# Kernel tuning notes

Measured on AMD Instinct MI355X. Metric: run time of the kernel, lower is better.

Reference implementation:

```python
import jax, jax.numpy as jnp
from jax import lax
import numpy as np

NSTART, NOPEN, NHID, NCLOSE, NLAYERS, KSZ, N = 40, 128, 256, 3, 40, 9, 1024
H_STEP = 0.1
PAD = (KSZ - 1) // 2  # 4 -> same-length conv
EPS = 1e-5


def conv1(x, K):
    # x: (1, Cin, N), K: (Cout, Cin, k); cross-correlation like torch F.conv1d
    return lax.conv_general_dilated(x, K, (1,), [(PAD, PAD)],
                                    dimension_numbers=('NCH', 'OIH', 'NCH'))


def conv1T(x, K):
    # torch F.conv_transpose1d(x, K, padding=PAD) == conv1d with swapped-channel,
    # flipped kernel and padding k-1-PAD (= PAD here since k=9, PAD=4)
    Kt = jnp.flip(jnp.swapaxes(K, 0, 1), -1)
    return lax.conv_general_dilated(x, Kt, (1,), [(PAD, PAD)],
                                    dimension_numbers=('NCH', 'OIH', 'NCH'))


def instance_norm(x):
    # x: (1, C, N); normalize per channel over spatial dim, biased var, no affine
    m = jnp.mean(x, axis=-1, keepdims=True)
    v = jnp.var(x, axis=-1, keepdims=True)
    return (x - m) * lax.rsqrt(v + EPS)


def get_graph_lap(Z):
    # Z: (C, N). Normalized Gaussian-affinity graph Laplacian.
    sq = jnp.sum(Z * Z, axis=0)  # (N,)
    D2 = jnp.maximum(sq[:, None] + sq[None, :] - 2.0 * (Z.T @ Z), 0.0)
    sigma = jnp.mean(D2) + 1e-12
    Wg = jnp.exp(-D2 / sigma)
    deg = jnp.sum(Wg, axis=1)
    Dh = lax.rsqrt(deg)
    L = Dh[:, None] * (jnp.diag(deg) - Wg) * Dh[None, :]
    return L, deg


def double_sym_layer(Z, Wi, Bi, L):
    # Z: (nopen, N), Wi: (2, nhid, nopen, 9), Bi: (2, nopen, 1), L: (N, N)
    A0 = instance_norm(conv1((Z + Bi[0])[None], Wi[0]))
    A1 = instance_norm((conv1((Z + Bi[1])[None], Wi[1])[0] @ L)[None])
    A0 = jax.nn.relu(A0)
    A1 = jax.nn.relu(A1)
    A0 = conv1T(A0, Wi[0])[0]
    A1 = conv1T(A1, Wi[1])[0] @ L.T
    return A0 + A1  # (nopen, N)


def setup_inputs() -> dict:
    key = jax.random.key(0)
    k1, k2, k3, k4, k5 = jax.random.split(key, 5)
    Z = jax.random.normal(k1, (NSTART, N), dtype=jnp.float32)
    stdv_o = 0.001 * NOPEN / NSTART
    Kopen = jax.random.uniform(k2, (NOPEN, NSTART), minval=-stdv_o, maxval=stdv_o, dtype=jnp.float32)
    stdv_c = 0.001 * NCLOSE / NOPEN
    Kclose = jax.random.uniform(k3, (NCLOSE, NOPEN), minval=-stdv_c, maxval=stdv_c, dtype=jnp.float32)
    W = jax.random.uniform(k4, (NLAYERS, 2, NHID, NOPEN, KSZ), minval=-1e-4, maxval=1e-4, dtype=jnp.float32)
    Bias = jax.random.uniform(k5, (NLAYERS, 2, NOPEN, 1), dtype=jnp.float32) * 1e-4
    return {"Z": Z, "Kopen": Kopen, "Kclose": Kclose, "W": W, "Bias": Bias}


def reference(Z, Kopen, Kclose, W, Bias):
    h = H_STEP
    Zc = Kopen @ Z          # (nopen, N)
    Zold = Zc
    L, _ = get_graph_lap(Zc)
    for i in range(NLAYERS):
        if i % 10 == 0:
            L, _ = get_graph_lap(Zc)
        Ai = double_sym_layer(Zc, W[i], Bias[i], L)
        Zc, Zold = 2.0 * Zc - Zold - (h * h) * Ai, Zc  # leapfrog step
    return (Kclose @ Zc, Kclose @ Zold)
```

## Files before the change

kernel.cpp:

```cpp
#include <hip/hip_runtime.h>

#define NN 1024
#define NOPEN 128
#define NHID 256
#define NSTART 40
#define NCLOSE 3
#define NLAYERS 40
#define KSZ 9

static constexpr float H2 = 0.01f;
static constexpr float IN_EPS = 1e-5f;

using floatx4 = __attribute__((ext_vector_type(4))) float;
using bfrag = __attribute__((ext_vector_type(8))) short;

__device__ __forceinline__ ushort f2bf(float f) {
    union { float f; unsigned u; } v; v.f = f;
    unsigned r = v.u + 0x7fffu + ((v.u >> 16) & 1u);
    return (ushort)(r >> 16);
}

__device__ __forceinline__ void prepw_piece(const float* __restrict__ W, ushort* __restrict__ Wt,
                                            ushort* __restrict__ WtT, int lb, int lsrc, int tid) {
    if (lb < 72) {
        int q = lb; int coq = q & 3; q >>= 2; int t = q % 9, z = q / 9;
        const float* Wz = W + (size_t)(lsrc * 2 + z) * (NHID * NOPEN * KSZ);
        ushort* Wo = Wt + ((size_t)z * 9 + t) * (NHID * NOPEN);
#pragma unroll
        for (int r = 0; r < 32; ++r) {
            int idx = r * 256 + tid;
            int co = coq * 64 + (idx >> 7), ci = idx & 127;
            Wo[co * NOPEN + ci] = f2bf(Wz[co * (NOPEN * KSZ) + ci * KSZ + t]);
        }
    } else {
        int q = lb - 72; int ciq = q & 3; q >>= 2; int t = q % 9, z = q / 9;
        const float* Wz = W + (size_t)(lsrc * 2 + z) * (NHID * NOPEN * KSZ);
        ushort* Wo = WtT + ((size_t)z * 9 + t) * (NOPEN * NHID);
#pragma unroll
        for (int r = 0; r < 32; ++r) {
            int idx = r * 256 + tid;
            int ci = ciq * 32 + (idx >> 8), co = idx & 255;
            Wo[ci * NHID + co] = f2bf(Wz[co * (NOPEN * KSZ) + ci * KSZ + t]);
        }
    }
}

__global__ __launch_bounds__(256) void k_open(const float* __restrict__ Kopen, const float* __restrict__ Z,
                       float* __restrict__ Zc, float* __restrict__ Zold,
                       const float* __restrict__ Bias0, ushort* __restrict__ Zct,
                       ushort* __restrict__ At0, ushort* __restrict__ At1,
                       const float* __restrict__ W, ushort* __restrict__ Wt,
                       ushort* __restrict__ WtT, float* __restrict__ sig) {
    const int v = blockIdx.x, tid = threadIdx.x;
    if (v < 512) {
        int o = v >> 2, n = (v & 3) * 256 + tid;
        float acc = 0.f;
#pragma unroll
        for (int s = 0; s < NSTART; ++s)
            acc = fmaf(Kopen[o * NSTART + s], Z[s * NN + n], acc);
        Zc[o * NN + n] = acc;
        Zold[o * NN + n] = acc;
#pragma unroll
        for (int z = 0; z < 2; ++z)
            Zct[z * (1032 * 128) + (n + 4) * 128 + o] = f2bf(acc + Bias0[z * NOPEN + o]);
    } else if (v < 656) {
        prepw_piece(W, Wt, WtT, v - 512, 0, tid);
    } else {
        if (tid == 0) sig[0] = 0.f;
        for (int idx = tid; idx < 1024; idx += 256) {
            int z = idx >> 9, rr = idx & 511;
            ushort* Zz = Zct + z * (1032 * 128);
            Zz[rr] = 0; Zz[1028 * 128 + rr] = 0;
        }
        for (int idx = tid; idx < 2048; idx += 256) {
            int a = idx >> 10, rr = idx & 1023;
            ushort* A = a ? At1 : At0;
            A[rr] = 0; A[1028 * 256 + rr] = 0;
        }
    }
}

__global__ __launch_bounds__(256) void k_d2(const float* __restrict__ Zc,
                                            float* __restrict__ D2, float* __restrict__ sig) {
    __shared__ __align__(16) float Zi[32 * 36];
    __shared__ __align__(16) float Zj[32 * 68];
    __shared__ float sqi[32], sqj[64];
    __shared__ float red[4];
    const int tid = threadIdx.x;
    const int tx = tid & 15, ty = tid >> 4;
    const int j0 = blockIdx.x * 64, i0 = blockIdx.y * 32;
    if (tid < 32) sqi[tid] = 0.f;
    else if (tid < 96) sqj[tid - 32] = 0.f;
    float acc[2][4] = {};
    for (int c0 = 0; c0 < NOPEN; c0 += 32) {
        for (int idx = tid; idx < 32 * 32; idx += 256) {
            int c = idx >> 5, ii = idx & 31;
            Zi[c * 36 + ii] = Zc[(c0 + c) * NN + i0 + ii];
        }
        for (int idx = tid; idx < 32 * 64; idx += 256) {
            int c = idx >> 6, jj = idx & 63;
            Zj[c * 68 + jj] = Zc[(c0 + c) * NN + j0 + jj];
        }
        __syncthreads();
        if (tid < 32) {
            float s = 0.f;
            for (int c = 0; c < 32; ++c) { float x = Zi[c * 36 + tid]; s = fmaf(x, x, s); }
            sqi[tid] += s;
        } else if (tid < 96) {
            int jj = tid - 32;
            float s = 0.f;
            for (int c = 0; c < 32; ++c) { float x = Zj[c * 68 + jj]; s = fmaf(x, x, s); }
            sqj[jj] += s;
        }
#pragma unroll 8
        for (int c = 0; c < 32; ++c) {
            float2 zi = *(const float2*)&Zi[c * 36 + ty * 2];
            float4 zj = *(const float4*)&Zj[c * 68 + tx * 4];
            acc[0][0] = fmaf(zi.x, zj.x, acc[0][0]);
            acc[0][1] = fmaf(zi.x, zj.y, acc[0][1]);
            acc[0][2] = fmaf(zi.x, zj.z, acc[0][2]);
            acc[0][3] = fmaf(zi.x, zj.w, acc[0][3]);
            acc[1][0] = fmaf(zi.y, zj.x, acc[1][0]);
            acc[1][1] = fmaf(zi.y, zj.y, acc[1][1]);
            acc[1][2] = fmaf(zi.y, zj.z, acc[1][2]);
            acc[1][3] = fmaf(zi.y, zj.w, acc[1][3]);
        }
        __syncthreads();
    }
    float part = 0.f;
#pragma unroll
    for (int m = 0; m < 2; ++m) {
        int i = i0 + ty * 2 + m;
        float sqi_v = sqi[ty * 2 + m];
        float4 d;
        d.x = fmaxf(sqi_v + sqj[tx * 4 + 0] - 2.f * acc[m][0], 0.f);
        d.y = fmaxf(sqi_v + sqj[tx * 4 + 1] - 2.f * acc[m][1], 0.f);
        d.z = fmaxf(sqi_v + sqj[tx * 4 + 2] - 2.f * acc[m][2], 0.f);
        d.w = fmaxf(sqi_v + sqj[tx * 4 + 3] - 2.f * acc[m][3], 0.f);
        *(float4*)&D2[(size_t)i * NN + j0 + tx * 4] = d;
        part += (d.x + d.y) + (d.z + d.w);
    }
#pragma unroll
    for (int off = 32; off > 0; off >>= 1) part += __shfl_down(part, off);
    if ((tid & 63) == 0) red[tid >> 6] = part;
    __syncthreads();
    if (tid == 0) atomicAdd(sig, red[0] + red[1] + red[2] + red[3]);
}

__global__ void k_deg(const float* __restrict__ D2, const float* __restrict__ sig,
                      float* __restrict__ Dh) {
    __shared__ float red[4];
    int i = blockIdx.x, tid = threadIdx.x;
    float inv = 1.f / (sig[0] * (1.f / 1048576.f) + 1e-12f);
    float4 v = *(const float4*)&D2[(size_t)i * NN + tid * 4];
    float s = __expf(-v.x * inv) + __expf(-v.y * inv) + __expf(-v.z * inv) + __expf(-v.w * inv);
#pragma unroll
    for (int off = 32; off > 0; off >>= 1) s += __shfl_down(s, off);
    if ((tid & 63) == 0) red[tid >> 6] = s;
    __syncthreads();
    if (tid == 0) Dh[i] = rsqrtf(red[0] + red[1] + red[2] + red[3]);
}

__global__ void k_L(const float* __restrict__ D2, const float* __restrict__ sig,
                    const float* __restrict__ Dh, ushort* __restrict__ Lb) {
    int i = blockIdx.x, tid = threadIdx.x;
    int j = tid * 4;
    float inv = 1.f / (sig[0] * (1.f / 1048576.f) + 1e-12f);
    float dhi = Dh[i];
    float4 v = *(const float4*)&D2[(size_t)i * NN + j];
    float4 dj = *(const float4*)&Dh[j];
    float4 o;
    o.x = -dhi * dj.x * __expf(-v.x * inv);
    o.y = -dhi * dj.y * __expf(-v.y * inv);
    o.z = -dhi * dj.z * __expf(-v.z * inv);
    o.w = -dhi * dj.w * __expf(-v.w * inv);
    if (i == j + 0) o.x += 1.f;
    if (i == j + 1) o.y += 1.f;
    if (i == j + 2) o.z += 1.f;
    if (i == j + 3) o.w += 1.f;
    ushort4 ob; ob.x = f2bf(o.x); ob.y = f2bf(o.y); ob.z = f2bf(o.z); ob.w = f2bf(o.w);
    *(ushort4*)&Lb[(size_t)i * NN + j] = ob;
}

__global__ __launch_bounds__(256) void k_conv(const ushort* __restrict__ Zct,
        const ushort* __restrict__ Wt, float* __restrict__ C0, ushort* __restrict__ C1b) {
    const int z = blockIdx.z;
    const int p0 = blockIdx.x * 64, co0 = blockIdx.y * 32;
    __shared__ ushort Xs[72 * 136];
    __shared__ ushort Wl[9 * 32 * 136];
    const int tid = threadIdx.x;
    const ushort* Zz = Zct + z * (1032 * 128);
    const ushort* Wz = Wt + (size_t)z * 9 * NHID * NOPEN;
    for (int idx = tid; idx < 1152; idx += 256) {
        int row = idx >> 4, ch = (idx & 15) * 8;
        *(bfrag*)&Xs[row * 136 + ch] = *(const bfrag*)&Zz[(p0 + row) * 128 + ch];
    }
    for (int idx = tid; idx < 4608; idx += 256) {
        int t = idx >> 9, rem = idx & 511;
        int c = rem >> 4, ch = (rem & 15) * 8;
        *(bfrag*)&Wl[(t * 32 + c) * 136 + ch] = *(const bfrag*)&Wz[(t * NHID + co0 + c) * 128 + ch];
    }
    __syncthreads();
    const int l = tid & 63, wv = tid >> 6;
    const int wm = wv >> 1, wn = wv & 1;
    const int lm = l & 15, lq = l >> 4;
    floatx4 acc[2] = {};
    for (int t = 0; t < 9; ++t) {
        const int wbase = (t * 32 + wm * 16 + lm) * 136 + lq * 8;
        const int xbase = (wn * 32 + lm + t) * 136 + lq * 8;
#pragma unroll
        for (int kc = 0; kc < 4; ++kc) {
            bfrag a = *(const bfrag*)&Wl[wbase + kc * 32];
            bfrag b0 = *(const bfrag*)&Xs[xbase + kc * 32];
            acc[0] = __builtin_amdgcn_mfma_f32_16x16x32_bf16(a, b0, acc[0], 0, 0, 0);
            bfrag b1 = *(const bfrag*)&Xs[xbase + 16 * 136 + kc * 32];
            acc[1] = __builtin_amdgcn_mfma_f32_16x16x32_bf16(a, b1, acc[1], 0, 0, 0);
        }
    }
    const int cog = co0 + wm * 16 + lq * 4;
    const int pg = p0 + wn * 32 + lm;
#pragma unroll
    for (int j = 0; j < 2; ++j)
#pragma unroll
        for (int r = 0; r < 4; ++r) {
            if (z == 0) C0[(cog + r) * NN + pg + j * 16] = acc[j][r];
            else        C1b[(cog + r) * NN + pg + j * 16] = f2bf(acc[j][r]);
        }
}

__global__ __launch_bounds__(256) void k_xl_mfma(const ushort* __restrict__ X,
                                                 const ushort* __restrict__ Lb,
                                                 float* __restrict__ P, int M) {
    __shared__ __align__(16) ushort As[64 * 136];
    __shared__ __align__(16) ushort Bs[128 * 136];
    const int tid = threadIdx.x;
    const int lane = tid & 63, wave = tid >> 6;
    const int wm = wave >> 1, wn = wave & 1;
    const int n0 = blockIdx.x * 128, m0 = blockIdx.y * 64, kc = blockIdx.z * 128;
    {
        int q = tid;
#pragma unroll
        for (int r = 0; r < 4; ++r, q += 256) {
            int row = q >> 4, ch = (q & 15) * 8;
            *(bfrag*)&As[row * 136 + ch] = *(const bfrag*)&X[(m0 + row) * NN + kc + ch];
        }
        q = tid;
#pragma unroll
        for (int r = 0; r < 8; ++r, q += 256) {
            int row = q >> 4, ch = (q & 15) * 8;
            *(bfrag*)&Bs[row * 136 + ch] = *(const bfrag*)&Lb[(n0 + row) * NN + kc + ch];
        }
    }
    __syncthreads();
    floatx4 acc[2][4] = {};
    const int lrow = (lane & 15) * 136;
    const int koff = (lane >> 4) * 8;
#pragma unroll
    for (int ks = 0; ks < 4; ++ks) {
        bfrag a[2], b[4];
#pragma unroll
        for (int i = 0; i < 2; ++i)
            a[i] = *(const bfrag*)&As[(wm * 32 + i * 16) * 136 + lrow + ks * 32 + koff];
#pragma unroll
        for (int j = 0; j < 4; ++j)
            b[j] = *(const bfrag*)&Bs[(wn * 64 + j * 16) * 136 + lrow + ks * 32 + koff];
#pragma unroll
        for (int i = 0; i < 2; ++i)
#pragma unroll
            for (int j = 0; j < 4; ++j)
                acc[i][j] = __builtin_amdgcn_mfma_f32_16x16x32_bf16(a[i], b[j], acc[i][j], 0, 0, 0);
    }
    const int mg0 = m0 + wm * 32 + (lane >> 4) * 4;
    const int ng0 = n0 + wn * 64 + (lane & 15);
    const size_t base = (size_t)blockIdx.z * M * NN;
#pragma unroll
    for (int i = 0; i < 2; ++i)
#pragma unroll
        for (int j = 0; j < 4; ++j)
#pragma unroll
            for (int r = 0; r < 4; ++r)
                P[base + (size_t)(mg0 + i * 16 + r) * NN + ng0 + j * 16] = acc[i][j][r];
}

__global__ void k_inorm(const float* __restrict__ C0, const float* __restrict__ P1,
                        float* __restrict__ A1sum, float* __restrict__ Mu, float* __restrict__ Rs) {
    const int c = blockIdx.x, arr = blockIdx.y, tid = threadIdx.x;
    __shared__ float rs[4], rq[4];
    float4 v;
    if (arr == 0) {
        v = *(const float4*)&C0[c * NN + tid * 4];
    } else {
        v.x = v.y = v.z = v.w = 0.f;
#pragma unroll
        for (int s = 0; s < 8; ++s) {
            float4 p = *(const float4*)&P1[(size_t)(s * NHID + c) * NN + tid * 4];
            v.x += p.x; v.y += p.y; v.z += p.z; v.w += p.w;
        }
        *(float4*)&A1sum[c * NN + tid * 4] = v;
    }
    float s = (v.x + v.y) + (v.z + v.w);
    float q = (v.x * v.x + v.y * v.y) + (v.z * v.z + v.w * v.w);
#pragma unroll
    for (int off = 32; off > 0; off >>= 1) { s += __shfl_down(s, off); q += __shfl_down(q, off); }
    if ((tid & 63) == 0) { rs[tid >> 6] = s; rq[tid >> 6] = q; }
    __syncthreads();
    if (tid == 0) {
        float S = rs[0] + rs[1] + rs[2] + rs[3];
        float Q = rq[0] + rq[1] + rq[2] + rq[3];
        float mean = S * (1.f / NN);
        float var = Q * (1.f / NN) - mean * mean;
        Mu[arr * NHID + c] = mean;
        Rs[arr * NHID + c] = rsqrtf(var + IN_EPS);
    }
}

__global__ __launch_bounds__(256) void k_normT(const float* __restrict__ C0,
        const float* __restrict__ A1sum, const float* __restrict__ Mu, const float* __restrict__ Rs,
        ushort* __restrict__ At0, ushort* __restrict__ At1) {
    const int arr = blockIdx.z;
    const int p0 = blockIdx.x * 64, co0 = blockIdx.y * 64;
    const float* in = arr ? A1sum : C0;
    ushort* out = arr ? At1 : At0;
    __shared__ ushort Ls[64 * 72];
    const int tid = threadIdx.x;
#pragma unroll
    for (int r = 0; r < 4; ++r) {
        int idx = r * 256 + tid;
        int col = idx >> 4, pq = idx & 15;
        int co = co0 + col;
        float4 v = *(const float4*)&in[(size_t)co * NN + p0 + pq * 4];
        float m = Mu[arr * NHID + co], sc = Rs[arr * NHID + co];
        Ls[(pq * 4 + 0) * 72 + col] = f2bf(fmaxf((v.x - m) * sc, 0.f));
        Ls[(pq * 4 + 1) * 72 + col] = f2bf(fmaxf((v.y - m) * sc, 0.f));
        Ls[(pq * 4 + 2) * 72 + col] = f2bf(fmaxf((v.z - m) * sc, 0.f));
        Ls[(pq * 4 + 3) * 72 + col] = f2bf(fmaxf((v.w - m) * sc, 0.f));
    }
    __syncthreads();
#pragma unroll
    for (int r = 0; r < 2; ++r) {
        int idx = r * 256 + tid;
        int row = idx >> 3, ch = (idx & 7) * 8;
        *(bfrag*)&out[(size_t)(p0 + row + 4) * 256 + co0 + ch] = *(const bfrag*)&Ls[row * 72 + ch];
    }
}

__global__ __launch_bounds__(256) void k_convT(const ushort* __restrict__ At0,
        const ushort* __restrict__ At1, const ushort* __restrict__ WtT,
        float* __restrict__ Tacc, ushort* __restrict__ T1b) {
    const int z = blockIdx.z;
    const int p0 = blockIdx.x * 64, ci0 = blockIdx.y * 16;
    __shared__ ushort Al[72 * 264];
    __shared__ ushort Wl[9 * 16 * 264];
    const ushort* A = z ? At1 : At0;
    const ushort* Wz = WtT + (size_t)z * 9 * NOPEN * NHID;
    const int tid = threadIdx.x;
    for (int idx = tid; idx < 2304; idx += 256) {
        int row = idx >> 5, ch = (idx & 31) * 8;
        *(bfrag*)&Al[row * 264 + ch] = *(const bfrag*)&A[(p0 + row) * 256 + ch];
    }
    for (int idx = tid; idx < 4608; idx += 256) {
        int t = idx >> 9, rem = idx & 511;
        int c = rem >> 5, ch = (rem & 31) * 8;
        *(bfrag*)&Wl[(t * 16 + c) * 264 + ch] = *(const bfrag*)&Wz[(t * NOPEN + ci0 + c) * 256 + ch];
    }
    __syncthreads();
    const int l = tid & 63, wv = tid >> 6;
    const int lm = l & 15, lq = l >> 4;
    floatx4 acc0 = {}, acc1 = {};
    for (int t = 0; t < 9; ++t) {
        const int abase = (wv * 16 + lm + 8 - t) * 264 + lq * 8;
        const int wbase = (t * 16 + lm) * 264 + lq * 8;
#pragma unroll
        for (int kc = 0; kc < 8; kc += 2) {
            bfrag a0 = *(const bfrag*)&Wl[wbase + kc * 32];
            bfrag b0 = *(const bfrag*)&Al[abase + kc * 32];
            acc0 = __builtin_amdgcn_mfma_f32_16x16x32_bf16(a0, b0, acc0, 0, 0, 0);
            bfrag a1 = *(const bfrag*)&Wl[wbase + kc * 32 + 32];
            bfrag b1 = *(const bfrag*)&Al[abase + kc * 32 + 32];
            acc1 = __builtin_amdgcn_mfma_f32_16x16x32_bf16(a1, b1, acc1, 0, 0, 0);
        }
    }
    floatx4 acc = acc0 + acc1;
    const int cig = ci0 + lq * 4;
    const int pg = p0 + wv * 16 + lm;
#pragma unroll
    for (int r = 0; r < 4; ++r) {
        if (z == 0) Tacc[(cig + r) * NN + pg] = acc[r];
        else        T1b[(cig + r) * NN + pg] = f2bf(acc[r]);
    }
}

__global__ __launch_bounds__(256) void k_leap(const float* __restrict__ P2,
        const float* __restrict__ Tacc, const float* __restrict__ Zc, float* __restrict__ Zo,
        const float* __restrict__ BiasN, ushort* __restrict__ Zct,
        const float* __restrict__ W, ushort* __restrict__ Wt, ushort* __restrict__ WtT,
        float* __restrict__ sig, int lnext, int doprep) {
    const int v = blockIdx.x, tid = threadIdx.x;
    if (v < 128) {
        int off = (v * 256 + tid) * 4;
        float4 a = *(const float4*)&Tacc[off];
#pragma unroll
        for (int s = 0; s < 8; ++s) {
            float4 p = *(const float4*)&P2[(size_t)(s << 17) + off];
            a.x += p.x; a.y += p.y; a.z += p.z; a.w += p.w;
        }
        float4 zc = *(const float4*)&Zc[off];
        float4 zo = *(const float4*)&Zo[off];
        float4 zn;
        zn.x = 2.f * zc.x - zo.x - H2 * a.x;
        zn.y = 2.f * zc.y - zo.y - H2 * a.y;
        zn.z = 2.f * zc.z - zo.z - H2 * a.z;
        zn.w = 2.f * zc.w - zo.w - H2 * a.w;
        *(float4*)&Zo[off] = zn;
        int ci = off >> 10, n = off & 1023;
#pragma unroll
        for (int z = 0; z < 2; ++z) {
            float bz = BiasN[z * NOPEN + ci];
            ushort* Zz = Zct + z * (1032 * 128);
            Zz[(n + 4) * 128 + ci] = f2bf(zn.x + bz);
            Zz[(n + 5) * 128 + ci] = f2bf(zn.y + bz);
            Zz[(n + 6) * 128 + ci] = f2bf(zn.z + bz);
            Zz[(n + 7) * 128 + ci] = f2bf(zn.w + bz);
        }
    } else if (v < 272) {
        if (doprep) prepw_piece(W, Wt, WtT, v - 128, lnext, tid);
    } else {
        if (tid == 0) sig[0] = 0.f;
    }
}

__global__ void k_close(const float* __restrict__ Kclose, const float* __restrict__ Zc,
                        const float* __restrict__ Zold, float* __restrict__ out) {
    int n = blockIdx.x * 256 + threadIdx.x;
    int o = blockIdx.y;
    const float* Zb = blockIdx.z ? Zold : Zc;
    float a = 0.f;
#pragma unroll
    for (int c = 0; c < NOPEN; ++c) a = fmaf(Kclose[o * NOPEN + c], Zb[c * NN + n], a);
    out[blockIdx.z * (NCLOSE * NN) + o * NN + n] = a;
}

extern "C" void kernel_launch(void* const* d_in, const int* in_sizes, int n_in,
                              void* d_out, int out_size, void* d_ws, size_t ws_size,
                              hipStream_t stream) {
    const float* Z      = (const float*)d_in[0];
    const float* Kopen  = (const float*)d_in[1];
    const float* Kclose = (const float*)d_in[2];
    const float* W      = (const float*)d_in[3];
    const float* Bias   = (const float*)d_in[4];
    float* out = (float*)d_out;
    float* ws  = (float*)d_ws;

    float* Zb0   = ws + 0;
    float* Zb1   = ws + 131072;
    float* D2    = ws + 262144;
    float* C0    = ws + 1310720;
    float* A1sum = ws + 1572864;
    float* Tacc  = ws + 1835008;
    float* P1    = ws + 1966080;
    float* P2    = ws + 4063232;
    float* Dh    = ws + 5111808;
    float* sig   = ws + 5112832;
    float* Mu    = ws + 5113856;
    float* Rs    = ws + 5114880;
    ushort* Lb  = (ushort*)(ws + 5115904);
    ushort* C1b = (ushort*)(ws + 5640192);
    ushort* T1b = (ushort*)(ws + 5771264);
    ushort* Zct = (ushort*)(ws + 5836800);
    ushort* At0 = (ushort*)(ws + 5968896);
    ushort* At1 = (ushort*)(ws + 6100992);
    ushort* Wt  = (ushort*)(ws + 6233088);
    ushort* WtT = (ushort*)(ws + 6528000);

    k_open<<<dim3(657), 256, 0, stream>>>(Kopen, Z, Zb0, Zb1, Bias, Zct, At0, At1,
                                          W, Wt, WtT, sig);

    float* Zc = Zb0;
    float* Zold = Zb1;
    for (int i = 0; i < NLAYERS; ++i) {
        if (i % 10 == 0) {
            k_d2<<<dim3(16, 32), 256, 0, stream>>>(Zc, D2, sig);
            k_deg<<<dim3(NN), 256, 0, stream>>>(D2, sig, Dh);
            k_L<<<dim3(NN), 256, 0, stream>>>(D2, sig, Dh, Lb);
        }
        k_conv<<<dim3(16, 8, 2), 256, 0, stream>>>(Zct, Wt, C0, C1b);
        k_xl_mfma<<<dim3(8, 4, 8), 256, 0, stream>>>(C1b, Lb, P1, NHID);
        k_inorm<<<dim3(NHID, 2), 256, 0, stream>>>(C0, P1, A1sum, Mu, Rs);
        k_normT<<<dim3(16, 4, 2), 256, 0, stream>>>(C0, A1sum, Mu, Rs, At0, At1);
        k_convT<<<dim3(16, 8, 2), 256, 0, stream>>>(At0, At1, WtT, Tacc, T1b);
        k_xl_mfma<<<dim3(8, 2, 8), 256, 0, stream>>>(T1b, Lb, P2, NOPEN);
        int lnext = (i + 1 < NLAYERS) ? i + 1 : NLAYERS - 1;
        k_leap<<<dim3(273), 256, 0, stream>>>(P2, Tacc, Zc, Zold,
                                              Bias + (size_t)lnext * 2 * NOPEN, Zct,
                                              W, Wt, WtT, sig, lnext, (i + 1 < NLAYERS) ? 1 : 0);
        float* tmp = Zc; Zc = Zold; Zold = tmp;
    }

    k_close<<<dim3(4, NCLOSE, 2), 256, 0, stream>>>(Kclose, Zc, Zold, out);
}
```

Measured before the change: 2.127 ms.

## Store conv weights in MFMA fragment order and reduce split-K with atomics

The conv and transposed-conv weights are now pre-swizzled into MFMA fragment order. Each wave loads its A fragments straight from global memory into registers, prefetching the next tap's fragments during the current tap's MFMAs, which removes the large shared-memory weight staging. The split-K graph-Laplacian GEMMs now atomically add into a single output buffer instead of writing eight partial slabs that later kernels summed. That output buffer (A1) is zeroed by extra blocks in the open and leap kernels. The trade-off is more atomic traffic, summation order that is no longer deterministic, and more register pressure from holding the prefetched fragments.

```diff
diff --git a/kernel.cpp b/kernel.cpp
--- a/kernel.cpp
+++ b/kernel.cpp
@@ -20,27 +20,38 @@
     return (ushort)(r >> 16);
 }
 
-__device__ __forceinline__ void prepw_piece(const float* __restrict__ W, ushort* __restrict__ Wt,
-                                            ushort* __restrict__ WtT, int lb, int lsrc, int tid) {
+__device__ __forceinline__ void prepw_piece(const float* __restrict__ W, ushort* __restrict__ Wf1,
+                                            ushort* __restrict__ Wf2, int lb, int lsrc, int tid) {
     if (lb < 72) {
-        int q = lb; int coq = q & 3; q >>= 2; int t = q % 9, z = q / 9;
+        int z = lb / 36, rem = lb % 36;
+        int t = rem >> 2, q = rem & 3;
         const float* Wz = W + (size_t)(lsrc * 2 + z) * (NHID * NOPEN * KSZ);
-        ushort* Wo = Wt + ((size_t)z * 9 + t) * (NHID * NOPEN);
+        ushort* dst = Wf1 + (((size_t)(z * 9 + t) * 64 + q * 16) << 9);
 #pragma unroll
         for (int r = 0; r < 32; ++r) {
-            int idx = r * 256 + tid;
-            int co = coq * 64 + (idx >> 7), ci = idx & 127;
-            Wo[co * NOPEN + ci] = f2bf(Wz[co * (NOPEN * KSZ) + ci * KSZ + t]);
+            int ei = r * 256 + tid;
+            int g = q * 4 + (ei >> 11);
+            int kc = (ei >> 9) & 3;
+            int lm = (ei >> 3) & 15, lq = (ei >> 7) & 3;
+            int e = ei & 7;
+            int co = g * 16 + lm, ci = kc * 32 + lq * 8 + e;
+            dst[ei] = f2bf(Wz[co * (NOPEN * KSZ) + ci * KSZ + t]);
         }
     } else {
-        int q = lb - 72; int ciq = q & 3; q >>= 2; int t = q % 9, z = q / 9;
+        int p2 = lb - 72;
+        int z = p2 / 36, rem = p2 % 36;
+        int t = rem >> 2, q = rem & 3;
         const float* Wz = W + (size_t)(lsrc * 2 + z) * (NHID * NOPEN * KSZ);
-        ushort* Wo = WtT + ((size_t)z * 9 + t) * (NOPEN * NHID);
+        ushort* dst = Wf2 + (((size_t)(z * 9 + t) * 64 + q * 16) << 9);
 #pragma unroll
         for (int r = 0; r < 32; ++r) {
-            int idx = r * 256 + tid;
-            int ci = ciq * 32 + (idx >> 8), co = idx & 255;
-            Wo[ci * NHID + co] = f2bf(Wz[co * (NOPEN * KSZ) + ci * KSZ + t]);
+            int ei = r * 256 + tid;
+            int fb = q * 16 + (ei >> 9);
+            int g = fb >> 3, j = fb & 7;
+            int lm = (ei >> 3) & 15, lq = (ei >> 7) & 3;
+            int e = ei & 7;
+            int ci = g * 16 + lm, co = j * 32 + lq * 8 + e;
+            dst[ei] = f2bf(Wz[co * (NOPEN * KSZ) + ci * KSZ + t]);
         }
     }
 }
@@ -49,8 +60,8 @@
                        float* __restrict__ Zc, float* __restrict__ Zold,
                        const float* __restrict__ Bias0, ushort* __restrict__ Zct,
                        ushort* __restrict__ At0, ushort* __restrict__ At1,
-                       const float* __restrict__ W, ushort* __restrict__ Wt,
-                       ushort* __restrict__ WtT, float* __restrict__ sig) {
+                       const float* __restrict__ W, ushort* __restrict__ Wf1,
+                       ushort* __restrict__ Wf2, float* __restrict__ sig, float* __restrict__ A1) {
     const int v = blockIdx.x, tid = threadIdx.x;
     if (v < 512) {
         int o = v >> 2, n = (v & 3) * 256 + tid;
@@ -64,8 +75,8 @@
         for (int z = 0; z < 2; ++z)
             Zct[z * (1032 * 128) + (n + 4) * 128 + o] = f2bf(acc + Bias0[z * NOPEN + o]);
     } else if (v < 656) {
-        prepw_piece(W, Wt, WtT, v - 512, 0, tid);
-    } else {
+        prepw_piece(W, Wf1, Wf2, v - 512, 0, tid);
+    } else if (v == 656) {
         if (tid == 0) sig[0] = 0.f;
         for (int idx = tid; idx < 1024; idx += 256) {
             int z = idx >> 9, rr = idx & 511;
@@ -77,6 +88,12 @@
             ushort* A = a ? At1 : At0;
             A[rr] = 0; A[1028 * 256 + rr] = 0;
         }
+    } else {
+        int b = v - 657;
+        size_t base = (size_t)b * 4096 + tid * 4;
+        float4 z4 = {0.f, 0.f, 0.f, 0.f};
+#pragma unroll
+        for (int r = 0; r < 4; ++r) *(float4*)&A1[base + r * 1024] = z4;
     }
 }
 
@@ -183,39 +200,42 @@
 }
 
 __global__ __launch_bounds__(256) void k_conv(const ushort* __restrict__ Zct,
-        const ushort* __restrict__ Wt, float* __restrict__ C0, ushort* __restrict__ C1b) {
+        const ushort* __restrict__ Wf1, float* __restrict__ C0, ushort* __restrict__ C1b) {
     const int z = blockIdx.z;
     const int p0 = blockIdx.x * 64, co0 = blockIdx.y * 32;
     __shared__ ushort Xs[72 * 136];
-    __shared__ ushort Wl[9 * 32 * 136];
     const int tid = threadIdx.x;
     const ushort* Zz = Zct + z * (1032 * 128);
-    const ushort* Wz = Wt + (size_t)z * 9 * NHID * NOPEN;
     for (int idx = tid; idx < 1152; idx += 256) {
         int row = idx >> 4, ch = (idx & 15) * 8;
         *(bfrag*)&Xs[row * 136 + ch] = *(const bfrag*)&Zz[(p0 + row) * 128 + ch];
     }
-    for (int idx = tid; idx < 4608; idx += 256) {
-        int t = idx >> 9, rem = idx & 511;
-        int c = rem >> 4, ch = (rem & 15) * 8;
-        *(bfrag*)&Wl[(t * 32 + c) * 136 + ch] = *(const bfrag*)&Wz[(t * NHID + co0 + c) * 128 + ch];
-    }
     __syncthreads();
     const int l = tid & 63, wv = tid >> 6;
     const int wm = wv >> 1, wn = wv & 1;
     const int lm = l & 15, lq = l >> 4;
+    const ushort* wf = Wf1 + (((size_t)z * 144 + (blockIdx.y * 2 + wm)) << 11) + l * 8;
     floatx4 acc[2] = {};
+    bfrag a_cur[4];
+#pragma unroll
+    for (int kc = 0; kc < 4; ++kc) a_cur[kc] = *(const bfrag*)(wf + (kc << 9));
     for (int t = 0; t < 9; ++t) {
-        const int wbase = (t * 32 + wm * 16 + lm) * 136 + lq * 8;
+        bfrag a_nxt[4];
+        if (t < 8) {
+            const ushort* wptr = wf + (size_t)(t + 1) * (16 << 11);
+#pragma unroll
+            for (int kc = 0; kc < 4; ++kc) a_nxt[kc] = *(const bfrag*)(wptr + (kc << 9));
+        }
         const int xbase = (wn * 32 + lm + t) * 136 + lq * 8;
 #pragma unroll
         for (int kc = 0; kc < 4; ++kc) {
-            bfrag a = *(const bfrag*)&Wl[wbase + kc * 32];
             bfrag b0 = *(const bfrag*)&Xs[xbase + kc * 32];
-            acc[0] = __builtin_amdgcn_mfma_f32_16x16x32_bf16(a, b0, acc[0], 0, 0, 0);
+            acc[0] = __builtin_amdgcn_mfma_f32_16x16x32_bf16(a_cur[kc], b0, acc[0], 0, 0, 0);
             bfrag b1 = *(const bfrag*)&Xs[xbase + 16 * 136 + kc * 32];
-            acc[1] = __builtin_amdgcn_mfma_f32_16x16x32_bf16(a, b1, acc[1], 0, 0, 0);
-        }
+            acc[1] = __builtin_amdgcn_mfma_f32_16x16x32_bf16(a_cur[kc], b1, acc[1], 0, 0, 0);
+        }
+#pragma unroll
+        for (int kc = 0; kc < 4; ++kc) a_cur[kc] = a_nxt[kc];
     }
     const int cog = co0 + wm * 16 + lq * 4;
     const int pg = p0 + wn * 32 + lm;
@@ -230,7 +250,7 @@
 
 __global__ __launch_bounds__(256) void k_xl_mfma(const ushort* __restrict__ X,
                                                  const ushort* __restrict__ Lb,
-                                                 float* __restrict__ P, int M) {
+                                                 float* __restrict__ Out) {
     __shared__ __align__(16) ushort As[64 * 136];
     __shared__ __align__(16) ushort Bs[128 * 136];
     const int tid = threadIdx.x;
@@ -272,32 +292,21 @@
     }
     const int mg0 = m0 + wm * 32 + (lane >> 4) * 4;
     const int ng0 = n0 + wn * 64 + (lane & 15);
-    const size_t base = (size_t)blockIdx.z * M * NN;
 #pragma unroll
     for (int i = 0; i < 2; ++i)
 #pragma unroll
         for (int j = 0; j < 4; ++j)
 #pragma unroll
             for (int r = 0; r < 4; ++r)
-                P[base + (size_t)(mg0 + i * 16 + r) * NN + ng0 + j * 16] = acc[i][j][r];
-}
-
-__global__ void k_inorm(const float* __restrict__ C0, const float* __restrict__ P1,
-                        float* __restrict__ A1sum, float* __restrict__ Mu, float* __restrict__ Rs) {
+                atomicAdd(&Out[(size_t)(mg0 + i * 16 + r) * NN + ng0 + j * 16], acc[i][j][r]);
+}
+
+__global__ void k_inorm(const float* __restrict__ C0, const float* __restrict__ A1,
+                        float* __restrict__ Mu, float* __restrict__ Rs) {
     const int c = blockIdx.x, arr = blockIdx.y, tid = threadIdx.x;
     __shared__ float rs[4], rq[4];
-    float4 v;
-    if (arr == 0) {
-        v = *(const float4*)&C0[c * NN + tid * 4];
-    } else {
-        v.x = v.y = v.z = v.w = 0.f;
-#pragma unroll
-        for (int s = 0; s < 8; ++s) {
-            float4 p = *(const float4*)&P1[(size_t)(s * NHID + c) * NN + tid * 4];
-            v.x += p.x; v.y += p.y; v.z += p.z; v.w += p.w;
-        }
-        *(float4*)&A1sum[c * NN + tid * 4] = v;
-    }
+    const float* in = arr ? A1 : C0;
+    float4 v = *(const float4*)&in[c * NN + tid * 4];
     float s = (v.x + v.y) + (v.z + v.w);
     float q = (v.x * v.x + v.y * v.y) + (v.z * v.z + v.w * v.w);
 #pragma unroll
@@ -315,11 +324,11 @@
 }
 
 __global__ __launch_bounds__(256) void k_normT(const float* __restrict__ C0,
-        const float* __restrict__ A1sum, const float* __restrict__ Mu, const float* __restrict__ Rs,
+        const float* __restrict__ A1, const float* __restrict__ Mu, const float* __restrict__ Rs,
         ushort* __restrict__ At0, ushort* __restrict__ At1) {
     const int arr = blockIdx.z;
     const int p0 = blockIdx.x * 64, co0 = blockIdx.y * 64;
-    const float* in = arr ? A1sum : C0;
+    const float* in = arr ? A1 : C0;
     ushort* out = arr ? At1 : At0;
     __shared__ ushort Ls[64 * 72];
     const int tid = threadIdx.x;
@@ -345,40 +354,42 @@
 }
 
 __global__ __launch_bounds__(256) void k_convT(const ushort* __restrict__ At0,
-        const ushort* __restrict__ At1, const ushort* __restrict__ WtT,
+        const ushort* __restrict__ At1, const ushort* __restrict__ Wf2,
         float* __restrict__ Tacc, ushort* __restrict__ T1b) {
     const int z = blockIdx.z;
     const int p0 = blockIdx.x * 64, ci0 = blockIdx.y * 16;
     __shared__ ushort Al[72 * 264];
-    __shared__ ushort Wl[9 * 16 * 264];
     const ushort* A = z ? At1 : At0;
-    const ushort* Wz = WtT + (size_t)z * 9 * NOPEN * NHID;
     const int tid = threadIdx.x;
     for (int idx = tid; idx < 2304; idx += 256) {
         int row = idx >> 5, ch = (idx & 31) * 8;
         *(bfrag*)&Al[row * 264 + ch] = *(const bfrag*)&A[(p0 + row) * 256 + ch];
     }
-    for (int idx = tid; idx < 4608; idx += 256) {
-        int t = idx >> 9, rem = idx & 511;
-        int c = rem >> 5, ch = (rem & 31) * 8;
-        *(bfrag*)&Wl[(t * 16 + c) * 264 + ch] = *(const bfrag*)&Wz[(t * NOPEN + ci0 + c) * 256 + ch];
-    }
     __syncthreads();
     const int l = tid & 63, wv = tid >> 6;
     const int lm = l & 15, lq = l >> 4;
+    const ushort* wf = Wf2 + (((size_t)z * 72 + blockIdx.y) << 12) + l * 8;
     floatx4 acc0 = {}, acc1 = {};
+    bfrag a_cur[8];
+#pragma unroll
+    for (int j = 0; j < 8; ++j) a_cur[j] = *(const bfrag*)(wf + (j << 9));
     for (int t = 0; t < 9; ++t) {
+        bfrag a_nxt[8];
+        if (t < 8) {
+            const ushort* wptr = wf + (size_t)(t + 1) * (8 << 12);
+#pragma unroll
+            for (int j = 0; j < 8; ++j) a_nxt[j] = *(const bfrag*)(wptr + (j << 9));
+        }
         const int abase = (wv * 16 + lm + 8 - t) * 264 + lq * 8;
-        const int wbase = (t * 16 + lm) * 264 + lq * 8;
-#pragma unroll
-        for (int kc = 0; kc < 8; kc += 2) {
-            bfrag a0 = *(const bfrag*)&Wl[wbase + kc * 32];
-            bfrag b0 = *(const bfrag*)&Al[abase + kc * 32];
-            acc0 = __builtin_amdgcn_mfma_f32_16x16x32_bf16(a0, b0, acc0, 0, 0, 0);
-            bfrag a1 = *(const bfrag*)&Wl[wbase + kc * 32 + 32];
-            bfrag b1 = *(const bfrag*)&Al[abase + kc * 32 + 32];
-            acc1 = __builtin_amdgcn_mfma_f32_16x16x32_bf16(a1, b1, acc1, 0, 0, 0);
-        }
+#pragma unroll
+        for (int j = 0; j < 8; j += 2) {
+            bfrag b0 = *(const bfrag*)&Al[abase + j * 32];
+            acc0 = __builtin_amdgcn_mfma_f32_16x16x32_bf16(a_cur[j], b0, acc0, 0, 0, 0);
+            bfrag b1 = *(const bfrag*)&Al[abase + j * 32 + 32];
+            acc1 = __builtin_amdgcn_mfma_f32_16x16x32_bf16(a_cur[j + 1], b1, acc1, 0, 0, 0);
+        }
+#pragma unroll
+        for (int j = 0; j < 8; ++j) a_cur[j] = a_nxt[j];
     }
     floatx4 acc = acc0 + acc1;
     const int cig = ci0 + lq * 4;
@@ -390,20 +401,15 @@
     }
 }
 
-__global__ __launch_bounds__(256) void k_leap(const float* __restrict__ P2,
-        const float* __restrict__ Tacc, const float* __restrict__ Zc, float* __restrict__ Zo,
+__global__ __launch_bounds__(256) void k_leap(const float* __restrict__ Tacc,
+        const float* __restrict__ Zc, float* __restrict__ Zo,
         const float* __restrict__ BiasN, ushort* __restrict__ Zct,
-        const float* __restrict__ W, ushort* __restrict__ Wt, ushort* __restrict__ WtT,
-        float* __restrict__ sig, int lnext, int doprep) {
+        const float* __restrict__ W, ushort* __restrict__ Wf1, ushort* __restrict__ Wf2,
+        float* __restrict__ A1, float* __restrict__ sig, int lnext, int doprep) {
     const int v = blockIdx.x, tid = threadIdx.x;
     if (v < 128) {
         int off = (v * 256 + tid) * 4;
         float4 a = *(const float4*)&Tacc[off];
-#pragma unroll
-        for (int s = 0; s < 8; ++s) {
-            float4 p = *(const float4*)&P2[(size_t)(s << 17) + off];
-            a.x += p.x; a.y += p.y; a.z += p.z; a.w += p.w;
-        }
         float4 zc = *(const float4*)&Zc[off];
         float4 zo = *(const float4*)&Zo[off];
         float4 zn;
@@ -423,9 +429,15 @@
             Zz[(n + 7) * 128 + ci] = f2bf(zn.w + bz);
         }
     } else if (v < 272) {
-        if (doprep) prepw_piece(W, Wt, WtT, v - 128, lnext, tid);
+        if (doprep) prepw_piece(W, Wf1, Wf2, v - 128, lnext, tid);
+    } else if (v == 272) {
+        if (tid == 0) sig[0] = 0.f;
     } else {
-        if (tid == 0) sig[0] = 0.f;
+        int b = v - 273;
+        size_t base = (size_t)b * 4096 + tid * 4;
+        float4 z4 = {0.f, 0.f, 0.f, 0.f};
+#pragma unroll
+        for (int r = 0; r < 4; ++r) *(float4*)&A1[base + r * 1024] = z4;
     }
 }
 
@@ -455,10 +467,8 @@
     float* Zb1   = ws + 131072;
     float* D2    = ws + 262144;
     float* C0    = ws + 1310720;
-    float* A1sum = ws + 1572864;
+    float* A1    = ws + 1572864;
     float* Tacc  = ws + 1835008;
-    float* P1    = ws + 1966080;
-    float* P2    = ws + 4063232;
     float* Dh    = ws + 5111808;
     float* sig   = ws + 5112832;
     float* Mu    = ws + 5113856;
@@ -469,11 +479,11 @@
     ushort* Zct = (ushort*)(ws + 5836800);
     ushort* At0 = (ushort*)(ws + 5968896);
     ushort* At1 = (ushort*)(ws + 6100992);
-    ushort* Wt  = (ushort*)(ws + 6233088);
-    ushort* WtT = (ushort*)(ws + 6528000);
-
-    k_open<<<dim3(657), 256, 0, stream>>>(Kopen, Z, Zb0, Zb1, Bias, Zct, At0, At1,
-                                          W, Wt, WtT, sig);
+    ushort* Wf1 = (ushort*)(ws + 6233088);
+    ushort* Wf2 = (ushort*)(ws + 6528000);
+
+    k_open<<<dim3(721), 256, 0, stream>>>(Kopen, Z, Zb0, Zb1, Bias, Zct, At0, At1,
+                                          W, Wf1, Wf2, sig, A1);
 
     float* Zc = Zb0;
     float* Zold = Zb1;
@@ -483,16 +493,16 @@
             k_deg<<<dim3(NN), 256, 0, stream>>>(D2, sig, Dh);
             k_L<<<dim3(NN), 256, 0, stream>>>(D2, sig, Dh, Lb);
         }
-        k_conv<<<dim3(16, 8, 2), 256, 0, stream>>>(Zct, Wt, C0, C1b);
-        k_xl_mfma<<<dim3(8, 4, 8), 256, 0, stream>>>(C1b, Lb, P1, NHID);
-        k_inorm<<<dim3(NHID, 2), 256, 0, stream>>>(C0, P1, A1sum, Mu, Rs);
-        k_normT<<<dim3(16, 4, 2), 256, 0, stream>>>(C0, A1sum, Mu, Rs, At0, At1);
-        k_convT<<<dim3(16, 8, 2), 256, 0, stream>>>(At0, At1, WtT, Tacc, T1b);
-        k_xl_mfma<<<dim3(8, 2, 8), 256, 0, stream>>>(T1b, Lb, P2, NOPEN);
+        k_conv<<<dim3(16, 8, 2), 256, 0, stream>>>(Zct, Wf1, C0, C1b);
+        k_xl_mfma<<<dim3(8, 4, 8), 256, 0, stream>>>(C1b, Lb, A1);
+        k_inorm<<<dim3(NHID, 2), 256, 0, stream>>>(C0, A1, Mu, Rs);
+        k_normT<<<dim3(16, 4, 2), 256, 0, stream>>>(C0, A1, Mu, Rs, At0, At1);
+        k_convT<<<dim3(16, 8, 2), 256, 0, stream>>>(At0, At1, Wf2, Tacc, T1b);
+        k_xl_mfma<<<dim3(8, 2, 8), 256, 0, stream>>>(T1b, Lb, Tacc);
         int lnext = (i + 1 < NLAYERS) ? i + 1 : NLAYERS - 1;
-        k_leap<<<dim3(273), 256, 0, stream>>>(P2, Tacc, Zc, Zold,
+        k_leap<<<dim3(337), 256, 0, stream>>>(Tacc, Zc, Zold,
                                               Bias + (size_t)lnext * 2 * NOPEN, Zct,
-                                              W, Wt, WtT, sig, lnext, (i + 1 < NLAYERS) ? 1 : 0);
+                                              W, Wf1, Wf2, A1, sig, lnext, (i + 1 < NLAYERS) ? 1 : 0);
         float* tmp = Zc; Zc = Zold; Zold = tmp;
     }
 
```

New measurement: 2.092 ms. Within noise of the previous version (-1.7%).
